# Optimization experiments

Hardware: AMD Instinct MI355X
Metric: run time of the kernel (lower is better)

Reference implementation:

```python
import jax, jax.numpy as jnp
import numpy as np

TOP_K = 4
NORM_TOPK_PROB = False  # Qwen2-MoE default

def setup_inputs() -> dict:
    key = jax.random.key(0)
    ks = jax.random.split(key, 10)
    B, S, D = 1, 2048, 2048
    E, F, FS = 8, 1408, 5632
    s = 0.02
    return {
        "hidden_states": jax.random.normal(ks[0], (B, S, D), jnp.float32),
        "gate_w": jax.random.normal(ks[1], (E, D), jnp.float32) * s,          # router Linear weight [E, D]
        "Wg": jax.random.normal(ks[2], (E, D, F), jnp.float32) * s,           # expert gate_proj
        "Wu": jax.random.normal(ks[3], (E, D, F), jnp.float32) * s,           # expert up_proj
        "Wd": jax.random.normal(ks[4], (E, F, D), jnp.float32) * s,           # expert down_proj
        "Wsg": jax.random.normal(ks[5], (D, FS), jnp.float32) * s,            # shared gate_proj
        "Wsu": jax.random.normal(ks[6], (D, FS), jnp.float32) * s,            # shared up_proj
        "Wsd": jax.random.normal(ks[7], (FS, D), jnp.float32) * s,            # shared down_proj
        "shared_gate_w": jax.random.normal(ks[8], (D, 1), jnp.float32) * s,   # shared_expert_gate Linear(D,1)
    }

def reference(hidden_states, gate_w, Wg, Wu, Wd, Wsg, Wsu, Wsd, shared_gate_w):
    B, S, D = hidden_states.shape
    x = hidden_states.reshape(-1, D)                       # [T, D]
    T = x.shape[0]
    router_logits = x @ gate_w.T                           # [T, E]
    probs = jax.nn.softmax(router_logits.astype(jnp.float32), axis=-1)
    top_vals, top_idx = jax.lax.top_k(probs, TOP_K)        # [T, K]
    if NORM_TOPK_PROB:
        top_vals = top_vals / jnp.sum(top_vals, axis=-1, keepdims=True)
    # dense routing-weight matrix: zero for unselected experts (same math as masked naive loop)
    w = jnp.zeros_like(probs).at[jnp.arange(T)[:, None], top_idx].set(top_vals)
    w = w.astype(x.dtype)                                  # [T, E]
    # per-expert SiLU-gated MLP, computed densely over all experts
    h = jax.nn.silu(jnp.einsum('td,edf->etf', x, Wg)) * jnp.einsum('td,edf->etf', x, Wu)  # [E, T, F]
    expert_out = jnp.einsum('etf,efd->etd', h, Wd)         # [E, T, D]
    moe_out = jnp.einsum('etd,te->td', expert_out, w)      # [T, D]
    # shared expert with sigmoid gate
    shared = (jax.nn.silu(x @ Wsg) * (x @ Wsu)) @ Wsd      # [T, D]
    shared = jax.nn.sigmoid(x @ shared_gate_w) * shared    # [T,1] * [T,D]
    out = (moe_out + shared).reshape(B, S, D)
    return out, router_logits
```

## Files before the change

kernel.cpp:

```cpp
#include <hip/hip_runtime.h>
#include <hip/hip_bf16.h>

typedef __attribute__((ext_vector_type(8))) __bf16 bf16x8;
typedef __attribute__((ext_vector_type(4))) float f32x4;

#define TKN 2048
#define DMODEL 2048
#define NEXP 8
#define FEXP 1408
#define FSH 5632

__device__ __forceinline__ unsigned short f2bf(float f) {
  unsigned u = __float_as_uint(f);
  u += 0x7FFFu + ((u >> 16) & 1u);
  return (unsigned short)(u >> 16);
}
__device__ __forceinline__ unsigned pk2(float a, float b) {
  return (unsigned)f2bf(a) | ((unsigned)f2bf(b) << 16);
}

__device__ __forceinline__ void gll16(const void* g, void* l) {
  __builtin_amdgcn_global_load_lds(
      (const __attribute__((address_space(1))) unsigned*)g,
      (__attribute__((address_space(3))) unsigned*)l, 16, 0, 0);
}

enum { EPI_GU = 0, EPI_DOWN = 1, EPI_SDOWN = 2 };

__global__ __launch_bounds__(256)
void router_k(const float* __restrict__ x, const float* __restrict__ gw,
              const float* __restrict__ sgw, float* __restrict__ logits,
              float* __restrict__ sig, int* __restrict__ cnt,
              int* __restrict__ tokl, float* __restrict__ wls)
{
  const int wv = threadIdx.x >> 6, lane = threadIdx.x & 63;
  const int t = blockIdx.x * 4 + wv;
  const float* xr = x + (long)t * DMODEL;
  float xv[32];
#pragma unroll
  for (int j = 0; j < 32; j++) xv[j] = xr[lane + (j << 6)];

  float lg[8];
#pragma unroll
  for (int e = 0; e < 8; e++) {
    const float* gr = gw + (long)e * DMODEL;
    float acc = 0.f;
#pragma unroll
    for (int j = 0; j < 32; j++) acc += xv[j] * gr[lane + (j << 6)];
#pragma unroll
    for (int s = 1; s < 64; s <<= 1) acc += __shfl_xor(acc, s, 64);
    lg[e] = acc;
  }
  float sgacc = 0.f;
#pragma unroll
  for (int j = 0; j < 32; j++) sgacc += xv[j] * sgw[lane + (j << 6)];
#pragma unroll
  for (int s = 1; s < 64; s <<= 1) sgacc += __shfl_xor(sgacc, s, 64);

  if (lane == 0) {
    float mx = lg[0];
#pragma unroll
    for (int e = 1; e < 8; e++) mx = fmaxf(mx, lg[e]);
    float p[8], se = 0.f;
#pragma unroll
    for (int e = 0; e < 8; e++) { p[e] = expf(lg[e] - mx); se += p[e]; }
    float inv = 1.f / se;
#pragma unroll
    for (int e = 0; e < 8; e++) { p[e] *= inv; logits[t * 8 + e] = lg[e]; }
    sig[t] = 1.f / (1.f + expf(-sgacc));
#pragma unroll
    for (int k = 0; k < 4; k++) {
      int bi = 0; float bv = p[0];
#pragma unroll
      for (int e = 1; e < 8; e++) if (p[e] > bv) { bv = p[e]; bi = e; }
      p[bi] = -1.f;
      int pos = atomicAdd(&cnt[bi], 1);
      tokl[bi * TKN + pos] = t;
      wls[bi * TKN + pos] = bv;
    }
  }
}

__global__ void scan_k(const int* __restrict__ cnt, int* __restrict__ offs) {
  if (threadIdx.x == 0) {
    int s = 0;
    for (int e = 0; e < 8; e++) { offs[e] = s; s += cnt[e]; }
    offs[8] = s;
  }
}

__global__ __launch_bounds__(256)
void cvt_x_k(const float* __restrict__ x, char* __restrict__ xbf)
{
  long id = (long)blockIdx.x * 256 + threadIdx.x;
  int row = id >> 8, u = id & 255, kt = u >> 2, j = u & 3;
  const float* p = x + (long)row * 2048 + kt * 32 + j * 4;
  float4 a = *(const float4*)p;
  float4 b = *(const float4*)(p + 16);
  uint4 o;
  o.x = pk2(a.x, a.y); o.y = pk2(a.z, a.w);
  o.z = pk2(b.x, b.y); o.w = pk2(b.z, b.w);
  *(uint4*)(xbf + id * 16) = o;
}

__global__ __launch_bounds__(256)
void cvt_w_k(const float* __restrict__ W, long sB, int N,
             char* __restrict__ panel, long panStride)
{
  const int ct = blockIdx.x, kt = blockIdx.y, e = blockIdx.z, KT = gridDim.y;
  const float* Wp = W + (long)e * sB + (long)(kt * 32) * N + ct * 128;
  __shared__ float t[32][128];
  const int r = threadIdx.x >> 3, q = threadIdx.x & 7;
  const float* rp = Wp + (long)r * N + q * 16;
  float4 f0 = *(const float4*)(rp + 0);
  float4 f1 = *(const float4*)(rp + 4);
  float4 f2 = *(const float4*)(rp + 8);
  float4 f3 = *(const float4*)(rp + 12);
  *(float4*)&t[r][q * 16 + 0]  = f0;
  *(float4*)&t[r][q * 16 + 4]  = f1;
  *(float4*)&t[r][q * 16 + 8]  = f2;
  *(float4*)&t[r][q * 16 + 12] = f3;
  __syncthreads();
  char* outp = panel + e * panStride + ((long)ct * KT + kt) * 8192;
#pragma unroll
  for (int uu = 0; uu < 2; uu++) {
    int u = threadIdx.x + uu * 256;
    int c = u >> 2;
    int g = (u & 3) ^ ((c >> 1) & 3);
    uint4 o;
    o.x = pk2(t[g * 4 + 0][c], t[g * 4 + 1][c]);
    o.y = pk2(t[g * 4 + 2][c], t[g * 4 + 3][c]);
    o.z = pk2(t[16 + g * 4 + 0][c], t[16 + g * 4 + 1][c]);
    o.w = pk2(t[16 + g * 4 + 2][c], t[16 + g * 4 + 3][c]);
    *(uint4*)(outp + u * 16) = o;
  }
}

__global__ __launch_bounds__(256)
void cvt_gu_k(const float* __restrict__ Wg, const float* __restrict__ Wu,
              long sB, int N, char* __restrict__ panel, long panStride)
{
  const int ct = blockIdx.x, kt = blockIdx.y, e = blockIdx.z, KT = gridDim.y;
  __shared__ float t[32][128];
  const int r = threadIdx.x >> 3, q = threadIdx.x & 7;
  const float* src = ((q >> 1) & 1) ? Wu : Wg;
  const int scol = ct * 64 + ((q >> 2) << 5) + ((q & 1) << 4);
  const float* rp = src + (long)e * sB + (long)(kt * 32 + r) * N + scol;
  float4 f0 = *(const float4*)(rp + 0);
  float4 f1 = *(const float4*)(rp + 4);
  float4 f2 = *(const float4*)(rp + 8);
  float4 f3 = *(const float4*)(rp + 12);
  *(float4*)&t[r][q * 16 + 0]  = f0;
  *(float4*)&t[r][q * 16 + 4]  = f1;
  *(float4*)&t[r][q * 16 + 8]  = f2;
  *(float4*)&t[r][q * 16 + 12] = f3;
  __syncthreads();
  char* outp = panel + e * panStride + ((long)ct * KT + kt) * 8192;
#pragma unroll
  for (int uu = 0; uu < 2; uu++) {
    int u = threadIdx.x + uu * 256;
    int c = u >> 2;
    int g = (u & 3) ^ ((c >> 1) & 3);
    uint4 o;
    o.x = pk2(t[g * 4 + 0][c], t[g * 4 + 1][c]);
    o.y = pk2(t[g * 4 + 2][c], t[g * 4 + 3][c]);
    o.z = pk2(t[16 + g * 4 + 0][c], t[16 + g * 4 + 1][c]);
    o.w = pk2(t[16 + g * 4 + 2][c], t[16 + g * 4 + 3][c]);
    *(uint4*)(outp + u * 16) = o;
  }
}

template<int EPI, bool EXPERT, int KSPLIT>
__global__ __launch_bounds__(256, 2)
void gemm2_k(const char* __restrict__ Abf, long strA,
             const char* __restrict__ Bp, long sBpan, int KTtot, int NCT,
             void* __restrict__ O, int ldKo,
             const int* __restrict__ cnt, const int* __restrict__ offs,
             const int* __restrict__ tokl, const float* __restrict__ wls,
             const float* __restrict__ sig)
{
  const int tid = threadIdx.x, lane = tid & 63, w = tid >> 6;
  const int wg = blockIdx.x;

  int e = 0, rt, ct, kc = 0, M = TKN;
  if (EXPERT) {
    e = wg & 7; int q = wg >> 3; rt = q & 15; ct = q >> 4;
    M = cnt[e];
    if (rt * 128 >= M) return;
  } else {
    rt = wg & 15; int q = wg >> 4; ct = q % NCT; kc = q / NCT;
  }
  const int KT = KTtot / KSPLIT;
  const int kt0 = kc * KT;
  const int obase = EXPERT ? offs[e] : 0;

  __shared__ int s_tok[128];
  __shared__ float s_w[128];
  __shared__ alignas(16) char Ab[3][8192];
  __shared__ alignas(16) char Bb[3][8192];

  if (EXPERT) {
    if (tid < 128) {
      int r = rt * 128 + tid;
      int rc = (r < M) ? r : (M - 1);
      s_tok[tid] = tokl[e * TKN + rc];
      if (EPI == EPI_DOWN) s_w[tid] = (r < M) ? wls[e * TKN + r] : 0.f;
    }
    __syncthreads();
  }

  const int lrow0 = w * 32 + (lane >> 2);
  const int lrow1 = lrow0 + 16;
  auto rowbyte = [&](int rl) -> long {
    long gr;
    if (EPI == EPI_DOWN) { int r = rt * 128 + rl; gr = obase + ((r < M) ? r : (M - 1)); }
    else if (EXPERT)     { gr = s_tok[rl]; }
    else                 { gr = rt * 128 + rl; }
    return gr * strA;
  };
  const int au0 = (lane & 3) ^ ((lrow0 >> 1) & 3);
  const int au1 = (lane & 3) ^ ((lrow1 >> 1) & 3);
  const char* gA0 = Abf + rowbyte(lrow0) + (long)kt0 * 64 + au0 * 16;
  const char* gA1 = Abf + rowbyte(lrow1) + (long)kt0 * 64 + au1 * 16;
  const long bbase = (EXPERT ? (long)e * sBpan : 0) + ((long)ct * KTtot + kt0) * 8192
                     + w * 2048 + (long)lane * 16;
  const char* gB = Bp + bbase;

  auto stage = [&](int bf, int kt) {
    long ao = (long)kt * 64, bo = (long)kt * 8192;
    gll16(gA0 + ao, &Ab[bf][w * 2048]);
    gll16(gA1 + ao, &Ab[bf][w * 2048 + 1024]);
    gll16(gB + bo, &Bb[bf][w * 2048]);
    gll16(gB + bo + 1024, &Bb[bf][w * 2048 + 1024]);
  };

  const int wm = w >> 1, wn = w & 1, g = lane >> 4, l15 = lane & 15;
  int raOff[4], rbOff[4];
#pragma unroll
  for (int m = 0; m < 4; m++) {
    int row = wm * 64 + m * 16 + l15;
    raOff[m] = row * 64 + ((g ^ ((row >> 1) & 3)) << 4);
  }
#pragma unroll
  for (int n = 0; n < 4; n++) {
    int col = wn * 64 + n * 16 + l15;
    rbOff[n] = col * 64 + ((g ^ ((col >> 1) & 3)) << 4);
  }

  f32x4 acc[4][4] = {};

  stage(0, 0);
  stage(1, 1);

  int rd = 0;
#pragma unroll 1
  for (int kt = 0; kt < KT; ++kt) {
    if (kt + 1 < KT) asm volatile("s_waitcnt vmcnt(4)" ::: "memory");
    else             asm volatile("s_waitcnt vmcnt(0)" ::: "memory");
    __builtin_amdgcn_s_barrier();
    __builtin_amdgcn_sched_barrier(0);

    bf16x8 av[4], bv[4];
#pragma unroll
    for (int m = 0; m < 4; m++) av[m] = *(const bf16x8*)&Ab[rd][raOff[m]];
#pragma unroll
    for (int n = 0; n < 4; n++) bv[n] = *(const bf16x8*)&Bb[rd][rbOff[n]];

    int wr = rd + 2; if (wr >= 3) wr -= 3;
    if (kt + 2 < KT) stage(wr, kt + 2);

    __builtin_amdgcn_s_setprio(1);
#pragma unroll
    for (int m = 0; m < 4; m++)
#pragma unroll
      for (int n = 0; n < 4; n++)
        acc[m][n] = __builtin_amdgcn_mfma_f32_16x16x32_bf16(av[m], bv[n], acc[m][n], 0, 0, 0);
    __builtin_amdgcn_s_setprio(0);
    __builtin_amdgcn_sched_barrier(0);
    rd = (rd == 2) ? 0 : rd + 1;
  }

  if constexpr (EPI == EPI_GU) {
#pragma unroll
    for (int m = 0; m < 4; m++) {
#pragma unroll
      for (int n = 0; n < 2; n++) {
        int lc = ct * 64 + wn * 32 + n * 16 + l15;
        f32x4 ga = acc[m][n];
        f32x4 ua = acc[m][n + 2];
#pragma unroll
        for (int q = 0; q < 4; q++) {
          int rl = wm * 64 + m * 16 + (g << 2) + q;
          int grow = rt * 128 + rl;
          if (!EXPERT || grow < M) {
            float gv = ga[q];
            float hv = (gv / (1.f + __expf(-gv))) * ua[q];
            long byteoff = (long)(obase + grow) * ((long)ldKo * 64)
                         + (lc >> 5) * 64 + ((lc >> 2) & 3) * 16
                         + ((lc & 16) >> 1) + (lc & 3) * 2;
            *(unsigned short*)((char*)O + byteoff) = f2bf(hv);
          }
        }
      }
    }
  } else {
#pragma unroll
    for (int m = 0; m < 4; m++) {
#pragma unroll
      for (int n = 0; n < 4; n++) {
        int col = ct * 128 + wn * 64 + n * 16 + l15;
        f32x4 a = acc[m][n];
#pragma unroll
        for (int q = 0; q < 4; q++) {
          int rl = wm * 64 + m * 16 + (g << 2) + q;
          int grow = rt * 128 + rl;
          float v = a[q];
          if constexpr (EPI == EPI_DOWN) {
            if (grow < M)
              atomicAdd((float*)O + (long)s_tok[rl] * DMODEL + col, s_w[rl] * v);
          } else {
            atomicAdd((float*)O + (long)grow * DMODEL + col, sig[grow] * v);
          }
        }
      }
    }
  }
}

__device__ __forceinline__ void block_sync_fb() {
  __builtin_amdgcn_sched_barrier(0);
  asm volatile("s_waitcnt lgkmcnt(0)" ::: "memory");
  __builtin_amdgcn_s_barrier();
  __builtin_amdgcn_sched_barrier(0);
}

template<int EPI, bool EXPERT, int KSPLIT>
__global__ __launch_bounds__(256, 2)
void gemm_fb_k(const float* __restrict__ A, int lda,
               const float* __restrict__ B, const float* __restrict__ B2,
               long sB, int ldb, int Ktot,
               float* __restrict__ O, int ldo,
               const int* __restrict__ cnt, const int* __restrict__ offs,
               const int* __restrict__ tokl, const float* __restrict__ wls,
               const float* __restrict__ sig)
{
  constexpr bool FUSED = (EPI == EPI_GU);
  const int tid = threadIdx.x;
  const int lane = tid & 63;

  int e = 0, rt, kc = 0, M = TKN;
  if (EXPERT) {
    e = blockIdx.y >> 4; rt = blockIdx.y & 15;
    M = cnt[e];
    if (rt * 128 >= M) return;
  } else {
    rt = blockIdx.y & 15; kc = blockIdx.y >> 4;
  }
  const int K = Ktot / KSPLIT;
  const int koff = kc * K;
  const int colblk = blockIdx.x * 128;
  const float* Bp  = B + (EXPERT ? (long)e * sB : 0);
  const float* Bp2 = FUSED ? (B2 + (EXPERT ? (long)e * sB : 0)) : nullptr;
  const int obase = EXPERT ? offs[e] : 0;

  __shared__ alignas(16) unsigned char Ab[8192];
  __shared__ alignas(16) unsigned char Bb[8192];
  __shared__ alignas(16) unsigned char Bb2[FUSED ? 8192 : 16];
  __shared__ int s_tok[128];
  __shared__ float s_w[128];

  if (EXPERT && tid < 128) {
    int r = rt * 128 + tid;
    int rc = (r < M) ? r : (M - 1);
    s_tok[tid] = tokl[e * TKN + rc];
    if (EPI == EPI_DOWN) s_w[tid] = (r < M) ? wls[e * TKN + r] : 0.f;
  }
  if (EXPERT) __syncthreads();

  const int arowl = tid >> 1;
  const int ahalf = tid & 1;
  long arow;
  if (EPI == EPI_DOWN) {
    int r = rt * 128 + arowl;
    arow = (long)obase + ((r < M) ? r : (M - 1));
  } else if (EXPERT) {
    arow = s_tok[arowl];
  } else {
    arow = rt * 128 + arowl;
  }
  const float* aptr = A + arow * (long)lda + koff + ahalf * 16;
  int wa[4];
#pragma unroll
  for (int j = 0; j < 4; j++)
    wa[j] = arowl * 64 + ((j ^ ((arowl ^ (arowl >> 3)) & 3)) << 4) + ahalf * 8;

  const int kg = tid >> 5, ng = tid & 31;
  const float* bptr  = Bp + (long)(koff + kg * 4) * ldb + colblk + ng * 4;
  const float* bptr2 = FUSED ? (Bp2 + (long)(koff + kg * 4) * ldb + colblk + ng * 4) : nullptr;
  int wb[4];
#pragma unroll
  for (int i = 0; i < 4; i++) {
    int c = ng * 4 + i;
    wb[i] = c * 64 + ((((kg & 3) ^ ((c ^ (c >> 3)) & 3))) << 4) + (kg >> 2) * 8;
  }

  const int wid = tid >> 6, wm = wid >> 1, wn = wid & 1;
  const int g = lane >> 4, l15 = lane & 15;
  int ra[4], rb[4];
#pragma unroll
  for (int m = 0; m < 4; m++) {
    int r = wm * 64 + m * 16 + l15;
    ra[m] = r * 64 + ((g ^ ((r ^ (r >> 3)) & 3)) << 4);
  }
#pragma unroll
  for (int n = 0; n < 4; n++) {
    int c = wn * 64 + n * 16 + l15;
    rb[n] = c * 64 + ((g ^ ((c ^ (c >> 3)) & 3)) << 4);
  }

  f32x4 acc[4][4] = {};
  f32x4 acc2[4][4] = {};

  const int KT = K >> 5;
  float4 ta0[4], tb0[4], tc0[4], ta1[4], tb1[4], tc1[4];

  auto load_tile = [&](float4* ra_, float4* rb_, float4* rc_, int kt) {
    const float4* a4 = reinterpret_cast<const float4*>(aptr + kt * 32);
    ra_[0] = a4[0]; ra_[1] = a4[1]; ra_[2] = a4[2]; ra_[3] = a4[3];
    const float* bb = bptr + (long)kt * 32 * ldb;
    rb_[0] = *reinterpret_cast<const float4*>(bb);
    rb_[1] = *reinterpret_cast<const float4*>(bb + ldb);
    rb_[2] = *reinterpret_cast<const float4*>(bb + 2 * ldb);
    rb_[3] = *reinterpret_cast<const float4*>(bb + 3 * ldb);
    if (FUSED) {
      const float* cc = bptr2 + (long)kt * 32 * ldb;
      rc_[0] = *reinterpret_cast<const float4*>(cc);
      rc_[1] = *reinterpret_cast<const float4*>(cc + ldb);
      rc_[2] = *reinterpret_cast<const float4*>(cc + 2 * ldb);
      rc_[3] = *reinterpret_cast<const float4*>(cc + 3 * ldb);
    }
  };

  auto store_tile = [&](const float4* ra_, const float4* rb_, const float4* rc_) {
#pragma unroll
    for (int j = 0; j < 4; j++)
      *reinterpret_cast<uint2*>(Ab + wa[j]) =
          make_uint2(pk2(ra_[j].x, ra_[j].y), pk2(ra_[j].z, ra_[j].w));
    *reinterpret_cast<uint2*>(Bb + wb[0]) = make_uint2(pk2(rb_[0].x, rb_[1].x), pk2(rb_[2].x, rb_[3].x));
    *reinterpret_cast<uint2*>(Bb + wb[1]) = make_uint2(pk2(rb_[0].y, rb_[1].y), pk2(rb_[2].y, rb_[3].y));
    *reinterpret_cast<uint2*>(Bb + wb[2]) = make_uint2(pk2(rb_[0].z, rb_[1].z), pk2(rb_[2].z, rb_[3].z));
    *reinterpret_cast<uint2*>(Bb + wb[3]) = make_uint2(pk2(rb_[0].w, rb_[1].w), pk2(rb_[2].w, rb_[3].w));
    if (FUSED) {
      *reinterpret_cast<uint2*>(Bb2 + wb[0]) = make_uint2(pk2(rc_[0].x, rc_[1].x), pk2(rc_[2].x, rc_[3].x));
      *reinterpret_cast<uint2*>(Bb2 + wb[1]) = make_uint2(pk2(rc_[0].y, rc_[1].y), pk2(rc_[2].y, rc_[3].y));
      *reinterpret_cast<uint2*>(Bb2 + wb[2]) = make_uint2(pk2(rc_[0].z, rc_[1].z), pk2(rc_[2].z, rc_[3].z));
      *reinterpret_cast<uint2*>(Bb2 + wb[3]) = make_uint2(pk2(rc_[0].w, rc_[1].w), pk2(rc_[2].w, rc_[3].w));
    }
  };

  auto mfma_step = [&]() {
    bf16x8 av[4], bvg[4], bvu[4];
#pragma unroll
    for (int m = 0; m < 4; m++) av[m] = *reinterpret_cast<const bf16x8*>(Ab + ra[m]);
#pragma unroll
    for (int n = 0; n < 4; n++) {
      bvg[n] = *reinterpret_cast<const bf16x8*>(Bb + rb[n]);
      if (FUSED) bvu[n] = *reinterpret_cast<const bf16x8*>(Bb2 + rb[n]);
    }
#pragma unroll
    for (int m = 0; m < 4; m++)
#pragma unroll
      for (int n = 0; n < 4; n++) {
        acc[m][n] = __builtin_amdgcn_mfma_f32_16x16x32_bf16(av[m], bvg[n], acc[m][n], 0, 0, 0);
        if (FUSED)
          acc2[m][n] = __builtin_amdgcn_mfma_f32_16x16x32_bf16(av[m], bvu[n], acc2[m][n], 0, 0, 0);
      }
  };

  load_tile(ta0, tb0, tc0, 0);
#pragma unroll 1
  for (int kt = 0; kt < KT; kt += 2) {
    load_tile(ta1, tb1, tc1, kt + 1);
    store_tile(ta0, tb0, tc0);
    block_sync_fb();
    mfma_step();
    block_sync_fb();
    int k2 = (kt + 2 < KT) ? kt + 2 : 0;
    load_tile(ta0, tb0, tc0, k2);
    store_tile(ta1, tb1, tc1);
    block_sync_fb();
    mfma_step();
    block_sync_fb();
  }

#pragma unroll
  for (int m = 0; m < 4; m++) {
#pragma unroll
    for (int n = 0; n < 4; n++) {
      int col = colblk + wn * 64 + n * 16 + l15;
      f32x4 a = acc[m][n];
      f32x4 a2 = acc2[m][n];
#pragma unroll
      for (int q = 0; q < 4; q++) {
        int rl = wm * 64 + m * 16 + (g << 2) + q;
        int grow = rt * 128 + rl;
        float v = a[q];
        if (EPI == EPI_GU) {
          if (!EXPERT || grow < M) {
            float hv = (v / (1.f + __expf(-v))) * a2[q];
            O[(long)(obase + grow) * ldo + col] = hv;
          }
        } else if (EPI == EPI_DOWN) {
          if (grow < M)
            atomicAdd(&O[(long)s_tok[rl] * ldo + col], s_w[rl] * v);
        } else {
          atomicAdd(&O[(long)grow * ldo + col], sig[grow] * v);
        }
      }
    }
  }
}

extern "C" void kernel_launch(void* const* d_in, const int* in_sizes, int n_in,
                              void* d_out, int out_size, void* d_ws, size_t ws_size,
                              hipStream_t stream)
{
  (void)in_sizes; (void)n_in; (void)out_size;
  const float* x   = (const float*)d_in[0];
  const float* gw  = (const float*)d_in[1];
  const float* Wg  = (const float*)d_in[2];
  const float* Wu  = (const float*)d_in[3];
  const float* Wd  = (const float*)d_in[4];
  const float* Wsg = (const float*)d_in[5];
  const float* Wsu = (const float*)d_in[6];
  const float* Wsd = (const float*)d_in[7];
  const float* sgw = (const float*)d_in[8];

  float* out    = (float*)d_out;
  float* logits = out + (long)TKN * DMODEL;

  char* w    = (char*)d_ws;
  int*  cnt  = (int*)w;
  int*  offs = (int*)(w + 64);
  float* sig = (float*)(w + 1024);
  int*  tokl = (int*)(w + 16384);
  float* wls = (float*)(w + 81920);

  hipMemsetAsync(out, 0, (size_t)TKN * DMODEL * 4, stream);
  hipMemsetAsync(cnt, 0, 64, stream);

  router_k<<<dim3(TKN / 4), 256, 0, stream>>>(x, gw, sgw, logits, sig, cnt, tokl, wls);
  scan_k<<<1, 64, 0, stream>>>(cnt, offs);

  const size_t NEED = 241172480ull;
  if (ws_size >= NEED) {
    char* xbf     = w + 262144;
    char* h       = w + 8650752;
    char* panGUex = w + 33554432;
    char* panWd   = w + 125829120;
    char* panGUsh = w + 171966464;
    char* panWsd  = w + 218103808;
    const long sPanGU = 11534336;
    const long sPanWd = 5767168;

    cvt_x_k<<<dim3(2048), 256, 0, stream>>>(x, xbf);
    cvt_gu_k<<<dim3(22, 64, 8), 256, 0, stream>>>(Wg, Wu, (long)DMODEL * FEXP, FEXP, panGUex, sPanGU);
    cvt_w_k<<<dim3(16, 44, 8), 256, 0, stream>>>(Wd, (long)FEXP * DMODEL, DMODEL, panWd, sPanWd);
    cvt_gu_k<<<dim3(88, 64, 1), 256, 0, stream>>>(Wsg, Wsu, 0, FSH, panGUsh, 0);
    cvt_w_k<<<dim3(16, 176, 1), 256, 0, stream>>>(Wsd, 0, DMODEL, panWsd, 0);

    gemm2_k<EPI_GU, true, 1><<<dim3(8 * 16 * 22), 256, 0, stream>>>(
        xbf, 4096, panGUex, sPanGU, 64, 22, h, 44, cnt, offs, tokl, wls, nullptr);
    gemm2_k<EPI_DOWN, true, 1><<<dim3(8 * 16 * 16), 256, 0, stream>>>(
        h, 2816, panWd, sPanWd, 44, 16, out, 0, cnt, offs, tokl, wls, nullptr);
    gemm2_k<EPI_GU, false, 1><<<dim3(16 * 88), 256, 0, stream>>>(
        xbf, 4096, panGUsh, 0, 64, 88, h, 176, nullptr, nullptr, nullptr, nullptr, nullptr);
    gemm2_k<EPI_SDOWN, false, 4><<<dim3(16 * 16 * 4), 256, 0, stream>>>(
        h, 11264, panWsd, 0, 176, 16, out, 0, nullptr, nullptr, nullptr, nullptr, sig);
  } else {
    float* h = (float*)(w + (1 << 20));
    gemm_fb_k<EPI_GU, true, 1><<<dim3(FEXP / 128, 128), 256, 0, stream>>>(
        x, DMODEL, Wg, Wu, (long)DMODEL * FEXP, FEXP, DMODEL, h, FEXP, cnt, offs, tokl, wls, nullptr);
    gemm_fb_k<EPI_DOWN, true, 1><<<dim3(DMODEL / 128, 128), 256, 0, stream>>>(
        h, FEXP, Wd, nullptr, (long)FEXP * DMODEL, DMODEL, FEXP, out, DMODEL, cnt, offs, tokl, wls, nullptr);
    gemm_fb_k<EPI_GU, false, 1><<<dim3(FSH / 128, TKN / 128), 256, 0, stream>>>(
        x, DMODEL, Wsg, Wsu, 0, FSH, DMODEL, h, FSH, nullptr, nullptr, nullptr, nullptr, nullptr);
    gemm_fb_k<EPI_SDOWN, false, 4><<<dim3(DMODEL / 128, (TKN / 128) * 4), 256, 0, stream>>>(
        h, FSH, Wsd, nullptr, 0, DMODEL, FSH, out, DMODEL, nullptr, nullptr, nullptr, nullptr, sig);
  }
}
```

Baseline: 679.8 us.

## Enlarge GEMM tiles to 256x256x64 with 512-thread blocks and matching panels

Replaces the 128x128x32 bf16 MFMA GEMM (256 threads, triple-buffered LDS) with a 256x256x64 tile using 512 threads, 8 waves each computing 128x64, and double-buffered 64KB-per-stage LDS. The weight-conversion kernels are rewritten to emit 256-column, 64-deep panels with a new 8-way XOR swizzle. The goal is more data reuse per loaded byte and fewer blocks. The cost is a larger LDS footprint that limits occupancy, shallower pipelining with a barrier per sub-step, and coarser tiles that waste work on partially filled expert row tiles and leave fewer blocks to spread across CUs.

```diff
diff --git a/kernel.cpp b/kernel.cpp
--- a/kernel.cpp
+++ b/kernel.cpp
@@ -104,75 +104,68 @@
 }
 
 __global__ __launch_bounds__(256)
-void cvt_w_k(const float* __restrict__ W, long sB, int N,
-             char* __restrict__ panel, long panStride)
-{
-  const int ct = blockIdx.x, kt = blockIdx.y, e = blockIdx.z, KT = gridDim.y;
-  const float* Wp = W + (long)e * sB + (long)(kt * 32) * N + ct * 128;
-  __shared__ float t[32][128];
-  const int r = threadIdx.x >> 3, q = threadIdx.x & 7;
-  const float* rp = Wp + (long)r * N + q * 16;
-  float4 f0 = *(const float4*)(rp + 0);
-  float4 f1 = *(const float4*)(rp + 4);
-  float4 f2 = *(const float4*)(rp + 8);
-  float4 f3 = *(const float4*)(rp + 12);
-  *(float4*)&t[r][q * 16 + 0]  = f0;
-  *(float4*)&t[r][q * 16 + 4]  = f1;
-  *(float4*)&t[r][q * 16 + 8]  = f2;
-  *(float4*)&t[r][q * 16 + 12] = f3;
+void cvt_w256_k(const float* __restrict__ W, long sB, int N,
+                char* __restrict__ panel, long panStride)
+{
+  const int ct4 = blockIdx.x, kt = blockIdx.y, e = blockIdx.z, KTT = gridDim.y;
+  __shared__ float t[64][65];
+  const int r = threadIdx.x >> 2, seg = threadIdx.x & 3;
+  const float* rp = W + (long)e * sB + (long)(kt * 64 + r) * N + ct4 * 64 + seg * 16;
+#pragma unroll
+  for (int i = 0; i < 4; i++)
+    *(float4*)&t[r][seg * 16 + i * 4] = *(const float4*)(rp + i * 4);
   __syncthreads();
-  char* outp = panel + e * panStride + ((long)ct * KT + kt) * 8192;
+  char* outp = panel + (long)e * panStride + ((long)(ct4 >> 2) * KTT + kt) * 32768;
 #pragma unroll
   for (int uu = 0; uu < 2; uu++) {
-    int u = threadIdx.x + uu * 256;
-    int c = u >> 2;
-    int g = (u & 3) ^ ((c >> 1) & 3);
+    int idx = threadIdx.x + uu * 256;
+    int cc = idx >> 3, u = idx & 7;
+    int cit = (ct4 & 3) * 64 + cc;
+    int gfr = u ^ (cit & 7);
+    int ks = gfr >> 2, j = gfr & 3;
     uint4 o;
-    o.x = pk2(t[g * 4 + 0][c], t[g * 4 + 1][c]);
-    o.y = pk2(t[g * 4 + 2][c], t[g * 4 + 3][c]);
-    o.z = pk2(t[16 + g * 4 + 0][c], t[16 + g * 4 + 1][c]);
-    o.w = pk2(t[16 + g * 4 + 2][c], t[16 + g * 4 + 3][c]);
-    *(uint4*)(outp + u * 16) = o;
+    o.x = pk2(t[ks * 32 + j * 4 + 0][cc], t[ks * 32 + j * 4 + 1][cc]);
+    o.y = pk2(t[ks * 32 + j * 4 + 2][cc], t[ks * 32 + j * 4 + 3][cc]);
+    o.z = pk2(t[ks * 32 + 16 + j * 4 + 0][cc], t[ks * 32 + 16 + j * 4 + 1][cc]);
+    o.w = pk2(t[ks * 32 + 16 + j * 4 + 2][cc], t[ks * 32 + 16 + j * 4 + 3][cc]);
+    *(uint4*)(outp + ((long)cit * 8 + u) * 16) = o;
   }
 }
 
 __global__ __launch_bounds__(256)
-void cvt_gu_k(const float* __restrict__ Wg, const float* __restrict__ Wu,
-              long sB, int N, char* __restrict__ panel, long panStride)
-{
-  const int ct = blockIdx.x, kt = blockIdx.y, e = blockIdx.z, KT = gridDim.y;
-  __shared__ float t[32][128];
-  const int r = threadIdx.x >> 3, q = threadIdx.x & 7;
-  const float* src = ((q >> 1) & 1) ? Wu : Wg;
-  const int scol = ct * 64 + ((q >> 2) << 5) + ((q & 1) << 4);
-  const float* rp = src + (long)e * sB + (long)(kt * 32 + r) * N + scol;
-  float4 f0 = *(const float4*)(rp + 0);
-  float4 f1 = *(const float4*)(rp + 4);
-  float4 f2 = *(const float4*)(rp + 8);
-  float4 f3 = *(const float4*)(rp + 12);
-  *(float4*)&t[r][q * 16 + 0]  = f0;
-  *(float4*)&t[r][q * 16 + 4]  = f1;
-  *(float4*)&t[r][q * 16 + 8]  = f2;
-  *(float4*)&t[r][q * 16 + 12] = f3;
+void cvt_gu256_k(const float* __restrict__ Wg, const float* __restrict__ Wu,
+                 long sB, int N, char* __restrict__ panel, long panStride)
+{
+  const int ct4 = blockIdx.x, kt = blockIdx.y, e = blockIdx.z, KTT = gridDim.y;
+  __shared__ float t[64][65];
+  const int r = threadIdx.x >> 2, seg = threadIdx.x & 3;
+  const float* src = (seg >= 2) ? Wu : Wg;
+  const float* rp = src + (long)e * sB + (long)(kt * 64 + r) * N
+                    + ct4 * 32 + (seg & 1) * 16;
+#pragma unroll
+  for (int i = 0; i < 4; i++)
+    *(float4*)&t[r][seg * 16 + i * 4] = *(const float4*)(rp + i * 4);
   __syncthreads();
-  char* outp = panel + e * panStride + ((long)ct * KT + kt) * 8192;
+  char* outp = panel + (long)e * panStride + ((long)(ct4 >> 2) * KTT + kt) * 32768;
 #pragma unroll
   for (int uu = 0; uu < 2; uu++) {
-    int u = threadIdx.x + uu * 256;
-    int c = u >> 2;
-    int g = (u & 3) ^ ((c >> 1) & 3);
+    int idx = threadIdx.x + uu * 256;
+    int cc = idx >> 3, u = idx & 7;
+    int cit = (ct4 & 3) * 64 + cc;
+    int gfr = u ^ (cit & 7);
+    int ks = gfr >> 2, j = gfr & 3;
     uint4 o;
-    o.x = pk2(t[g * 4 + 0][c], t[g * 4 + 1][c]);
-    o.y = pk2(t[g * 4 + 2][c], t[g * 4 + 3][c]);
-    o.z = pk2(t[16 + g * 4 + 0][c], t[16 + g * 4 + 1][c]);
-    o.w = pk2(t[16 + g * 4 + 2][c], t[16 + g * 4 + 3][c]);
-    *(uint4*)(outp + u * 16) = o;
+    o.x = pk2(t[ks * 32 + j * 4 + 0][cc], t[ks * 32 + j * 4 + 1][cc]);
+    o.y = pk2(t[ks * 32 + j * 4 + 2][cc], t[ks * 32 + j * 4 + 3][cc]);
+    o.z = pk2(t[ks * 32 + 16 + j * 4 + 0][cc], t[ks * 32 + 16 + j * 4 + 1][cc]);
+    o.w = pk2(t[ks * 32 + 16 + j * 4 + 2][cc], t[ks * 32 + 16 + j * 4 + 3][cc]);
+    *(uint4*)(outp + ((long)cit * 8 + u) * 16) = o;
   }
 }
 
 template<int EPI, bool EXPERT, int KSPLIT>
-__global__ __launch_bounds__(256, 2)
-void gemm2_k(const char* __restrict__ Abf, long strA,
+__global__ __launch_bounds__(512, 2)
+void gemm3_k(const char* __restrict__ Abf, long strA,
              const char* __restrict__ Bp, long sBpan, int KTtot, int NCT,
              void* __restrict__ O, int ldKo,
              const int* __restrict__ cnt, const int* __restrict__ offs,
@@ -184,24 +177,24 @@
 
   int e = 0, rt, ct, kc = 0, M = TKN;
   if (EXPERT) {
-    e = wg & 7; int q = wg >> 3; rt = q & 15; ct = q >> 4;
+    e = wg & 7; int q = wg >> 3; rt = q & 7; ct = q >> 3;
     M = cnt[e];
-    if (rt * 128 >= M) return;
+    if (rt * 256 >= M) return;
   } else {
-    rt = wg & 15; int q = wg >> 4; ct = q % NCT; kc = q / NCT;
+    rt = wg & 7; int q = wg >> 3; ct = q % NCT; kc = q / NCT;
   }
   const int KT = KTtot / KSPLIT;
   const int kt0 = kc * KT;
   const int obase = EXPERT ? offs[e] : 0;
 
-  __shared__ int s_tok[128];
-  __shared__ float s_w[128];
-  __shared__ alignas(16) char Ab[3][8192];
-  __shared__ alignas(16) char Bb[3][8192];
+  __shared__ int s_tok[256];
+  __shared__ float s_w[256];
+  __shared__ alignas(16) char Ab[2][32768];
+  __shared__ alignas(16) char Bb[2][32768];
 
   if (EXPERT) {
-    if (tid < 128) {
-      int r = rt * 128 + tid;
+    if (tid < 256) {
+      int r = rt * 256 + tid;
       int rc = (r < M) ? r : (M - 1);
       s_tok[tid] = tokl[e * TKN + rc];
       if (EPI == EPI_DOWN) s_w[tid] = (r < M) ? wls[e * TKN + r] : 0.f;
@@ -209,89 +202,104 @@
     __syncthreads();
   }
 
-  const int lrow0 = w * 32 + (lane >> 2);
-  const int lrow1 = lrow0 + 16;
   auto rowbyte = [&](int rl) -> long {
     long gr;
-    if (EPI == EPI_DOWN) { int r = rt * 128 + rl; gr = obase + ((r < M) ? r : (M - 1)); }
+    if (EPI == EPI_DOWN) { int r = rt * 256 + rl; gr = obase + ((r < M) ? r : (M - 1)); }
     else if (EXPERT)     { gr = s_tok[rl]; }
-    else                 { gr = rt * 128 + rl; }
+    else                 { gr = rt * 256 + rl; }
     return gr * strA;
   };
-  const int au0 = (lane & 3) ^ ((lrow0 >> 1) & 3);
-  const int au1 = (lane & 3) ^ ((lrow1 >> 1) & 3);
-  const char* gA0 = Abf + rowbyte(lrow0) + (long)kt0 * 64 + au0 * 16;
-  const char* gA1 = Abf + rowbyte(lrow1) + (long)kt0 * 64 + au1 * 16;
-  const long bbase = (EXPERT ? (long)e * sBpan : 0) + ((long)ct * KTtot + kt0) * 8192
-                     + w * 2048 + (long)lane * 16;
-  const char* gB = Bp + bbase;
+  const int su = (lane & 7) ^ ((lane >> 3) & 7);
+  const char* gA[4];
+#pragma unroll
+  for (int i = 0; i < 4; i++) {
+    int lr = (w * 4 + i) * 8 + (lane >> 3);
+    gA[i] = Abf + rowbyte(lr) + (long)kt0 * 128 + su * 16;
+  }
+  const char* gB = Bp + (EXPERT ? (long)e * sBpan : 0)
+                 + ((long)ct * KTtot + kt0) * 32768;
 
   auto stage = [&](int bf, int kt) {
-    long ao = (long)kt * 64, bo = (long)kt * 8192;
-    gll16(gA0 + ao, &Ab[bf][w * 2048]);
-    gll16(gA1 + ao, &Ab[bf][w * 2048 + 1024]);
-    gll16(gB + bo, &Bb[bf][w * 2048]);
-    gll16(gB + bo + 1024, &Bb[bf][w * 2048 + 1024]);
+    long ao = (long)kt * 128, bo = (long)kt * 32768;
+#pragma unroll
+    for (int i = 0; i < 4; i++)
+      gll16(gA[i] + ao, &Ab[bf][(w * 4 + i) * 1024]);
+#pragma unroll
+    for (int i = 0; i < 4; i++)
+      gll16(gB + bo + (w * 4 + i) * 1024 + (long)lane * 16,
+            &Bb[bf][(w * 4 + i) * 1024]);
   };
 
-  const int wm = w >> 1, wn = w & 1, g = lane >> 4, l15 = lane & 15;
-  int raOff[4], rbOff[4];
-#pragma unroll
-  for (int m = 0; m < 4; m++) {
-    int row = wm * 64 + m * 16 + l15;
-    raOff[m] = row * 64 + ((g ^ ((row >> 1) & 3)) << 4);
-  }
-#pragma unroll
-  for (int n = 0; n < 4; n++) {
-    int col = wn * 64 + n * 16 + l15;
-    rbOff[n] = col * 64 + ((g ^ ((col >> 1) & 3)) << 4);
-  }
-
-  f32x4 acc[4][4] = {};
+  const int wm = w >> 2, wn = w & 3, g = lane >> 4, l15 = lane & 15;
+  const int sw = l15 & 7;
+  int rbOff[2][4];
+#pragma unroll
+  for (int ks = 0; ks < 2; ks++)
+#pragma unroll
+    for (int n = 0; n < 4; n++) {
+      int col = wn * 64 + n * 16 + l15;
+      rbOff[ks][n] = col * 128 + (((ks * 4 + g) ^ sw) << 4);
+    }
+
+  f32x4 acc[8][4] = {};
 
   stage(0, 0);
-  stage(1, 1);
-
-  int rd = 0;
+  asm volatile("s_waitcnt vmcnt(0)" ::: "memory");
+  __builtin_amdgcn_s_barrier();
+  __builtin_amdgcn_sched_barrier(0);
+
 #pragma unroll 1
   for (int kt = 0; kt < KT; ++kt) {
-    if (kt + 1 < KT) asm volatile("s_waitcnt vmcnt(4)" ::: "memory");
-    else             asm volatile("s_waitcnt vmcnt(0)" ::: "memory");
-    __builtin_amdgcn_s_barrier();
-    __builtin_amdgcn_sched_barrier(0);
-
-    bf16x8 av[4], bv[4];
-#pragma unroll
-    for (int m = 0; m < 4; m++) av[m] = *(const bf16x8*)&Ab[rd][raOff[m]];
-#pragma unroll
-    for (int n = 0; n < 4; n++) bv[n] = *(const bf16x8*)&Bb[rd][rbOff[n]];
-
-    int wr = rd + 2; if (wr >= 3) wr -= 3;
-    if (kt + 2 < KT) stage(wr, kt + 2);
-
-    __builtin_amdgcn_s_setprio(1);
-#pragma unroll
-    for (int m = 0; m < 4; m++)
+    const int cur = kt & 1;
+    if (kt + 1 < KT) stage(cur ^ 1, kt + 1);
+
+    bf16x8 bv[2][4];
+#pragma unroll
+    for (int ks = 0; ks < 2; ks++)
 #pragma unroll
       for (int n = 0; n < 4; n++)
-        acc[m][n] = __builtin_amdgcn_mfma_f32_16x16x32_bf16(av[m], bv[n], acc[m][n], 0, 0, 0);
-    __builtin_amdgcn_s_setprio(0);
-    __builtin_amdgcn_sched_barrier(0);
-    rd = (rd == 2) ? 0 : rd + 1;
+        bv[ks][n] = *(const bf16x8*)&Bb[cur][rbOff[ks][n]];
+
+#pragma unroll
+    for (int p = 0; p < 4; p++) {
+      bf16x8 av[2][2];
+#pragma unroll
+      for (int mi = 0; mi < 2; mi++) {
+        int row = wm * 128 + (p * 2 + mi) * 16 + l15;
+#pragma unroll
+        for (int ks = 0; ks < 2; ks++)
+          av[mi][ks] = *(const bf16x8*)&Ab[cur][row * 128 + (((ks * 4 + g) ^ sw) << 4)];
+      }
+      __builtin_amdgcn_sched_barrier(0);
+      __builtin_amdgcn_s_setprio(1);
+#pragma unroll
+      for (int ks = 0; ks < 2; ks++)
+#pragma unroll
+        for (int n = 0; n < 4; n++)
+#pragma unroll
+          for (int mi = 0; mi < 2; mi++)
+            acc[p * 2 + mi][n] = __builtin_amdgcn_mfma_f32_16x16x32_bf16(
+                av[mi][ks], bv[ks][n], acc[p * 2 + mi][n], 0, 0, 0);
+      __builtin_amdgcn_s_setprio(0);
+      __builtin_amdgcn_sched_barrier(0);
+      if (p == 3)
+        asm volatile("s_waitcnt vmcnt(0)" ::: "memory");
+      __builtin_amdgcn_s_barrier();
+    }
   }
 
   if constexpr (EPI == EPI_GU) {
 #pragma unroll
-    for (int m = 0; m < 4; m++) {
+    for (int mm = 0; mm < 8; mm++) {
 #pragma unroll
       for (int n = 0; n < 2; n++) {
-        int lc = ct * 64 + wn * 32 + n * 16 + l15;
-        f32x4 ga = acc[m][n];
-        f32x4 ua = acc[m][n + 2];
+        int lc = ct * 128 + wn * 32 + n * 16 + l15;
+        f32x4 ga = acc[mm][n];
+        f32x4 ua = acc[mm][n + 2];
 #pragma unroll
         for (int q = 0; q < 4; q++) {
-          int rl = wm * 64 + m * 16 + (g << 2) + q;
-          int grow = rt * 128 + rl;
+          int rl = wm * 128 + mm * 16 + (g << 2) + q;
+          int grow = rt * 256 + rl;
           if (!EXPERT || grow < M) {
             float gv = ga[q];
             float hv = (gv / (1.f + __expf(-gv))) * ua[q];
@@ -305,15 +313,15 @@
     }
   } else {
 #pragma unroll
-    for (int m = 0; m < 4; m++) {
+    for (int mm = 0; mm < 8; mm++) {
 #pragma unroll
       for (int n = 0; n < 4; n++) {
-        int col = ct * 128 + wn * 64 + n * 16 + l15;
-        f32x4 a = acc[m][n];
+        int col = ct * 256 + wn * 64 + n * 16 + l15;
+        f32x4 a = acc[mm][n];
 #pragma unroll
         for (int q = 0; q < 4; q++) {
-          int rl = wm * 64 + m * 16 + (g << 2) + q;
-          int grow = rt * 128 + rl;
+          int rl = wm * 128 + mm * 16 + (g << 2) + q;
+          int grow = rt * 256 + rl;
           float v = a[q];
           if constexpr (EPI == EPI_DOWN) {
             if (grow < M)
@@ -564,19 +572,19 @@
     const long sPanWd = 5767168;
 
     cvt_x_k<<<dim3(2048), 256, 0, stream>>>(x, xbf);
-    cvt_gu_k<<<dim3(22, 64, 8), 256, 0, stream>>>(Wg, Wu, (long)DMODEL * FEXP, FEXP, panGUex, sPanGU);
-    cvt_w_k<<<dim3(16, 44, 8), 256, 0, stream>>>(Wd, (long)FEXP * DMODEL, DMODEL, panWd, sPanWd);
-    cvt_gu_k<<<dim3(88, 64, 1), 256, 0, stream>>>(Wsg, Wsu, 0, FSH, panGUsh, 0);
-    cvt_w_k<<<dim3(16, 176, 1), 256, 0, stream>>>(Wsd, 0, DMODEL, panWsd, 0);
-
-    gemm2_k<EPI_GU, true, 1><<<dim3(8 * 16 * 22), 256, 0, stream>>>(
-        xbf, 4096, panGUex, sPanGU, 64, 22, h, 44, cnt, offs, tokl, wls, nullptr);
-    gemm2_k<EPI_DOWN, true, 1><<<dim3(8 * 16 * 16), 256, 0, stream>>>(
-        h, 2816, panWd, sPanWd, 44, 16, out, 0, cnt, offs, tokl, wls, nullptr);
-    gemm2_k<EPI_GU, false, 1><<<dim3(16 * 88), 256, 0, stream>>>(
-        xbf, 4096, panGUsh, 0, 64, 88, h, 176, nullptr, nullptr, nullptr, nullptr, nullptr);
-    gemm2_k<EPI_SDOWN, false, 4><<<dim3(16 * 16 * 4), 256, 0, stream>>>(
-        h, 11264, panWsd, 0, 176, 16, out, 0, nullptr, nullptr, nullptr, nullptr, sig);
+    cvt_gu256_k<<<dim3(44, 32, 8), 256, 0, stream>>>(Wg, Wu, (long)DMODEL * FEXP, FEXP, panGUex, sPanGU);
+    cvt_w256_k<<<dim3(32, 22, 8), 256, 0, stream>>>(Wd, (long)FEXP * DMODEL, DMODEL, panWd, sPanWd);
+    cvt_gu256_k<<<dim3(176, 32, 1), 256, 0, stream>>>(Wsg, Wsu, 0, FSH, panGUsh, 0);
+    cvt_w256_k<<<dim3(32, 88, 1), 256, 0, stream>>>(Wsd, 0, DMODEL, panWsd, 0);
+
+    gemm3_k<EPI_GU, true, 1><<<dim3(8 * 8 * 11), 512, 0, stream>>>(
+        xbf, 4096, panGUex, sPanGU, 32, 11, h, 44, cnt, offs, tokl, wls, nullptr);
+    gemm3_k<EPI_DOWN, true, 1><<<dim3(8 * 8 * 8), 512, 0, stream>>>(
+        h, 2816, panWd, sPanWd, 22, 8, out, 0, cnt, offs, tokl, wls, nullptr);
+    gemm3_k<EPI_GU, false, 1><<<dim3(8 * 44), 512, 0, stream>>>(
+        xbf, 4096, panGUsh, 0, 32, 44, h, 176, nullptr, nullptr, nullptr, nullptr, nullptr);
+    gemm3_k<EPI_SDOWN, false, 4><<<dim3(8 * 8 * 4), 512, 0, stream>>>(
+        h, 11264, panWsd, 0, 88, 8, out, 0, nullptr, nullptr, nullptr, nullptr, sig);
   } else {
     float* h = (float*)(w + (1 << 20));
     gemm_fb_k<EPI_GU, true, 1><<<dim3(FEXP / 128, 128), 256, 0, stream>>>(
```

After: 872.8 us. +28.4%, slower.
